# Kernel optimization log

Measured on AMD Instinct MI355X. Metric: run time of the kernel, lower is better.

The kernel has to match this reference:

```python
import jax, jax.numpy as jnp
import numpy as np

# Grid / model dims
B, H, W = 1, 90, 180
P = H * W                 # 16200 spatial points
MODEL_DIM = 130
L = MODEL_DIM - 2         # learnable_dim = 128
NH, HD = 8, 16            # n_heads, head_dim
S = 16                    # shared_hidden (DISCO out_channels)
K = 25                    # number of DISCO basis functions (piecewise-linear 5x5)
NNB = 25                  # neighbors per output point (theta_cutoff stencil)
MH = 32                   # head MLP hidden
FH = 256                  # FFN hidden


def setup_inputs() -> dict:
    key = jax.random.key(0)
    ks = jax.random.split(key, 12)
    x = jax.random.normal(ks[0], (B, H, W, MODEL_DIM), dtype=jnp.float32)
    # sparse DISCO structure: neighbor indices + precomputed (quadrature-weighted) basis values
    nbr_idx = jax.random.randint(ks[1], (P, NNB), 0, P, dtype=jnp.int32)
    basis_vals = jax.random.normal(ks[2], (K, P, NNB), dtype=jnp.float32) * 0.1
    # learnable DISCO kernel weights (out_channels=S, in_channels=1, K basis coeffs) + bias
    disco_w = jax.random.normal(ks[3], (S, K), dtype=jnp.float32) / np.sqrt(K).astype(np.float32)
    disco_b = jax.random.normal(ks[4], (S,), dtype=jnp.float32) * 0.01
    # per-head MLP params: S -> MH -> 1, one set per head
    head_w1 = jax.random.normal(ks[5], (NH, S, MH), dtype=jnp.float32) / np.sqrt(S).astype(np.float32)
    head_b1 = jnp.zeros((NH, MH), dtype=jnp.float32)
    head_w2 = jax.random.normal(ks[6], (NH, MH, 1), dtype=jnp.float32) / np.sqrt(MH).astype(np.float32)
    head_b2 = jnp.zeros((NH, 1), dtype=jnp.float32)
    # FFN: model_dim -> FH -> L, with the sin/cos input columns zeroed (as in __init__)
    ffn_w1 = jax.random.normal(ks[7], (MODEL_DIM, FH), dtype=jnp.float32) / np.sqrt(MODEL_DIM).astype(np.float32)
    ffn_w1 = ffn_w1.at[-2:, :].set(0.0)
    ffn_b1 = jnp.zeros((FH,), dtype=jnp.float32)
    ffn_w2 = jax.random.normal(ks[8], (FH, L), dtype=jnp.float32) / np.sqrt(FH).astype(np.float32)
    ffn_b2 = jnp.zeros((L,), dtype=jnp.float32)
    return dict(x=x, nbr_idx=nbr_idx, basis_vals=basis_vals, disco_w=disco_w, disco_b=disco_b,
                head_w1=head_w1, head_b1=head_b1, head_w2=head_w2, head_b2=head_b2,
                ffn_w1=ffn_w1, ffn_b1=ffn_b1, ffn_w2=ffn_w2, ffn_b2=ffn_b2)


def reference(x, nbr_idx, basis_vals, disco_w, disco_b,
              head_w1, head_b1, head_w2, head_b2,
              ffn_w1, ffn_b1, ffn_w2, ffn_b2):
    gelu = lambda t: jax.nn.gelu(t, approximate=False)  # torch nn.GELU default is exact
    x_learn = x[..., :L]          # (B,H,W,L)
    sin_cos = x[..., L:]          # (B,H,W,2)
    x_res = x_learn

    # ---- DISCO spherical conv, depthwise over B*L channels (in_channels=1) ----
    xf = jnp.transpose(x_learn, (0, 3, 1, 2)).reshape(B * L, P)      # (N, P)
    gathered = xf[:, nbr_idx]                                        # (N, P, NNB) irregular gather
    z = jnp.einsum('kpn,cpn->ckp', basis_vals, gathered)             # (N, K, P) basis projections
    y = jnp.einsum('sk,ckp->csp', disco_w, z) + disco_b[None, :, None]  # (N, S, P)
    disco_out = y.reshape(B, L, S, H, W).transpose(0, 3, 4, 1, 2)    # (B,H,W,L,S)

    # ---- per-head MLP, vectorized over heads ----
    hfeat = disco_out.reshape(B, H, W, NH, HD, S)                    # (B,H,W,NH,HD,S)
    h1 = gelu(jnp.einsum('bxyhds,hsm->bxyhdm', hfeat, head_w1) + head_b1[:, None, :])
    hout = jnp.einsum('bxyhdm,hmo->bxyhdo', h1, head_w2) + head_b2[:, None, :]  # o=1
    x_mix = hout.reshape(B, H, W, L)                                 # heads concatenated in order
    x_mix = x_mix + x_res                                            # residual

    # ---- FFN channel mixing on [x_mix, sin_cos] ----
    x_full = jnp.concatenate([x_mix, sin_cos], axis=-1)              # (B,H,W,MODEL_DIM)
    hf = gelu(jnp.einsum('bxyd,df->bxyf', x_full, ffn_w1) + ffn_b1)
    x_ffn = jnp.einsum('bxyf,fl->bxyl', hf, ffn_w2) + ffn_b2
    x_out = x_ffn + x_mix
    return jnp.concatenate([x_out, sin_cos], axis=-1)                # (B,H,W,MODEL_DIM)
```

## Files before the change

### kernel.cpp

```cpp
#include <hip/hip_runtime.h>
#include <hip/hip_bf16.h>

#define P_TOT 16200
#define MODEL_DIMC 130
#define L_DIM 128
#define NHH 8
#define S_DIM 16
#define K_DIM 25
#define NNBC 25
#define MH_DIM 32
#define FH_DIM 256

__device__ __forceinline__ float gelu_f(float x) {
    float z = fabsf(x) * 0.70710678118654752440f;
    float t = __builtin_amdgcn_rcpf(fmaf(0.3275911f, z, 1.0f));
    float poly = t * fmaf(t, fmaf(t, fmaf(t, fmaf(t, 1.061405429f, -1.453152027f),
                                          1.421413741f), -0.284496736f), 0.254829592f);
    float e = __expf(-z * z);
    float erfp = fmaf(-poly, e, 1.0f);
    float erfv = copysignf(erfp, x);
    return 0.5f * x * (1.0f + erfv);
}

#define NB1 1583
__global__ __launch_bounds__(256) void k1_bw_t(const float* __restrict__ basis,
                                               const float* __restrict__ disco_w,
                                               const float* __restrict__ hw1,
                                               float* __restrict__ bw,
                                               float* __restrict__ w1t) {
    int bid = blockIdx.x;
    int tid = threadIdx.x;
    if (bid >= NB1) {
        int i = (bid - NB1) * 256 + tid;
        if (i < NHH * S_DIM * MH_DIM) {
            int h = i >> 9, s = (i >> 5) & 15, m = i & 31;
            w1t[h * 512 + m * 16 + s] = hw1[i];
        }
        return;
    }
    __shared__ float w[S_DIM * K_DIM];
    for (int i = tid; i < S_DIM * K_DIM; i += 256) w[i] = disco_w[i];
    __syncthreads();
    int i = bid * 256 + tid;
    if (i >= P_TOT * NNBC) return;
    float bv[K_DIM];
#pragma unroll
    for (int k = 0; k < K_DIM; k++) bv[k] = basis[k * (P_TOT * NNBC) + i];
    float acc[S_DIM];
#pragma unroll
    for (int s = 0; s < S_DIM; s++) {
        float a = 0.f;
#pragma unroll
        for (int k = 0; k < K_DIM; k++) a = fmaf(w[s * K_DIM + k], bv[k], a);
        acc[s] = a;
    }
    float4* outp = (float4*)(bw + (size_t)i * S_DIM);
#pragma unroll
    for (int q = 0; q < 4; q++) {
        float4 v; v.x = acc[q*4+0]; v.y = acc[q*4+1]; v.z = acc[q*4+2]; v.w = acc[q*4+3];
        outp[q] = v;
    }
}

__global__ __launch_bounds__(256, 5) void k2_disco_head(
        const float* __restrict__ x, const int* __restrict__ nbr,
        const float* __restrict__ bw, const float* __restrict__ w1t,
        const float* __restrict__ head_b1, const float* __restrict__ head_w2,
        const float* __restrict__ head_b2, const float* __restrict__ disco_b,
        float* __restrict__ xmix) {
    __shared__ float ylds[4 * 2048];

    int tid  = threadIdx.x;
    int lane = tid & 63;
    int wv   = __builtin_amdgcn_readfirstlane(tid >> 6);
    int p0   = blockIdx.x * 4;
    int p    = p0 + wv;

    const float* bwp = bw + (size_t)p * (NNBC * S_DIM);
    const int*   nbp = nbr + p * NNBC;

    float y0[16], y1[16];
#pragma unroll
    for (int s = 0; s < 16; s++) { float db = disco_b[s]; y0[s] = db; y1[s] = db; }

    const float* xb0 = x + lane;
    const float* xb1 = x + 64 + lane;

#pragma unroll 1
    for (int nb = 0; nb < 24; nb += 2) {
        int u0 = nbp[nb], u1 = nbp[nb + 1];
        float g00 = xb0[(size_t)u0 * MODEL_DIMC];
        float g01 = xb1[(size_t)u0 * MODEL_DIMC];
        float g10 = xb0[(size_t)u1 * MODEL_DIMC];
        float g11 = xb1[(size_t)u1 * MODEL_DIMC];
#pragma unroll
        for (int s = 0; s < 16; s++) {
            float w0  = bwp[nb * 16 + s];
            float w1_ = bwp[nb * 16 + 16 + s];
            y0[s] = fmaf(g00, w0, y0[s]);
            y1[s] = fmaf(g01, w0, y1[s]);
            y0[s] = fmaf(g10, w1_, y0[s]);
            y1[s] = fmaf(g11, w1_, y1[s]);
        }
    }
    {
        int u = nbp[24];
        float g0 = xb0[(size_t)u * MODEL_DIMC];
        float g1 = xb1[(size_t)u * MODEL_DIMC];
#pragma unroll
        for (int s = 0; s < 16; s++) {
            float wv_ = bwp[24 * 16 + s];
            y0[s] = fmaf(g0, wv_, y0[s]);
            y1[s] = fmaf(g1, wv_, y1[s]);
        }
    }

    int cr0 = (lane + 8 * wv) & 127;
    int cr1 = (cr0 + 64) & 127;
#pragma unroll
    for (int s = 0; s < 16; s++) {
        ylds[wv * 2048 + s * 128 + cr0] = y0[s];
        ylds[wv * 2048 + s * 128 + cr1] = y1[s];
    }
    __syncthreads();

    int ptl = lane >> 4;
    int d   = lane & 15;
    int ybase = ptl * 2048;
    int rot   = 8 * ptl;
#pragma unroll
    for (int t = 0; t < 2; t++) {
        int hh = __builtin_amdgcn_readfirstlane(wv + 4 * t);
        int cc  = hh * 16 + d;
        int col = (cc + rot) & 127;
        float yv[16];
#pragma unroll
        for (int s = 0; s < 16; s++)
            yv[s] = ylds[ybase + s * 128 + col];
        const float* wrow = w1t + hh * (MH_DIM * S_DIM);
        const float* b1r  = head_b1 + hh * MH_DIM;
        const float* w2r  = head_w2 + hh * MH_DIM;
        float acc = head_b2[hh];
#pragma unroll 1
        for (int m = 0; m < MH_DIM; m += 2) {
            const float* wm0 = wrow + m * 16;
            const float* wm1 = wrow + m * 16 + 16;
            float a0 = b1r[m], a1 = b1r[m + 1];
            float a0b = 0.f, a1b = 0.f;
#pragma unroll
            for (int s = 0; s < 8; s++) {
                a0  = fmaf(yv[s],     wm0[s],     a0);
                a0b = fmaf(yv[s + 8], wm0[s + 8], a0b);
                a1  = fmaf(yv[s],     wm1[s],     a1);
                a1b = fmaf(yv[s + 8], wm1[s + 8], a1b);
            }
            a0 += a0b; a1 += a1b;
            a0 = gelu_f(a0);
            a1 = gelu_f(a1);
            acc = fmaf(a0, w2r[m],     acc);
            acc = fmaf(a1, w2r[m + 1], acc);
        }
        int pp = p0 + ptl;
        xmix[pp * L_DIM + cc] = acc + x[(size_t)pp * MODEL_DIMC + cc];
    }
}

__global__ __launch_bounds__(256) void k3_ffn(
        const float* __restrict__ x, const float* __restrict__ xmix,
        const float* __restrict__ w1, const float* __restrict__ b1,
        const float* __restrict__ w2, const float* __restrict__ b2,
        float* __restrict__ out) {
    __shared__ __align__(16) float xm[16 * 132];
    __shared__ __align__(16) float hfl[16 * 260];
    int tid = threadIdx.x;
    int p0 = blockIdx.x * 16;
    int valid = min(16, P_TOT - p0);
    {
        const float4* src = (const float4*)(xmix + (size_t)p0 * L_DIM);
        for (int j = tid; j < valid * 32; j += 256) {
            float4 v = src[j];
            int pt = j >> 5, q = j & 31;
            *(float4*)&xm[pt * 132 + q * 4] = v;
        }
    }
    __syncthreads();

    {
        int fid = tid & 63, wid = tid >> 6;
        int f0 = fid * 4;
        float4 bb = *(const float4*)&b1[f0];
        float acc[4][4];
#pragma unroll
        for (int i = 0; i < 4; i++) {
            acc[i][0] = bb.x; acc[i][1] = bb.y; acc[i][2] = bb.z; acc[i][3] = bb.w;
        }
#pragma unroll 2
        for (int k0 = 0; k0 < 128; k0 += 4) {
            float4 w4[4];
#pragma unroll
            for (int j = 0; j < 4; j++)
                w4[j] = *(const float4*)&w1[(k0 + j) * FH_DIM + f0];
#pragma unroll
            for (int i = 0; i < 4; i++) {
                float4 xv = *(const float4*)&xm[(wid * 4 + i) * 132 + k0];
                acc[i][0] = fmaf(xv.x, w4[0].x, acc[i][0]);
                acc[i][1] = fmaf(xv.x, w4[0].y, acc[i][1]);
                acc[i][2] = fmaf(xv.x, w4[0].z, acc[i][2]);
                acc[i][3] = fmaf(xv.x, w4[0].w, acc[i][3]);
                acc[i][0] = fmaf(xv.y, w4[1].x, acc[i][0]);
                acc[i][1] = fmaf(xv.y, w4[1].y, acc[i][1]);
                acc[i][2] = fmaf(xv.y, w4[1].z, acc[i][2]);
                acc[i][3] = fmaf(xv.y, w4[1].w, acc[i][3]);
                acc[i][0] = fmaf(xv.z, w4[2].x, acc[i][0]);
                acc[i][1] = fmaf(xv.z, w4[2].y, acc[i][1]);
                acc[i][2] = fmaf(xv.z, w4[2].z, acc[i][2]);
                acc[i][3] = fmaf(xv.z, w4[2].w, acc[i][3]);
                acc[i][0] = fmaf(xv.w, w4[3].x, acc[i][0]);
                acc[i][1] = fmaf(xv.w, w4[3].y, acc[i][1]);
                acc[i][2] = fmaf(xv.w, w4[3].z, acc[i][2]);
                acc[i][3] = fmaf(xv.w, w4[3].w, acc[i][3]);
            }
        }
#pragma unroll
        for (int i = 0; i < 4; i++) {
            int pt = wid * 4 + i;
            float4 v;
            v.x = gelu_f(acc[i][0]);
            v.y = gelu_f(acc[i][1]);
            v.z = gelu_f(acc[i][2]);
            v.w = gelu_f(acc[i][3]);
            *(float4*)&hfl[pt * 260 + f0] = v;
        }
    }
    __syncthreads();

    {
        int lid = tid & 31, pgb = tid >> 5;
        int l0 = lid * 4;
        float4 bb = *(const float4*)&b2[l0];
        float acc[2][4];
#pragma unroll
        for (int i = 0; i < 2; i++) {
            acc[i][0] = bb.x; acc[i][1] = bb.y; acc[i][2] = bb.z; acc[i][3] = bb.w;
        }
#pragma unroll 2
        for (int f0 = 0; f0 < FH_DIM; f0 += 4) {
            float4 w4[4];
#pragma unroll
            for (int j = 0; j < 4; j++)
                w4[j] = *(const float4*)&w2[(f0 + j) * L_DIM + l0];
#pragma unroll
            for (int i = 0; i < 2; i++) {
                float4 hv = *(const float4*)&hfl[(pgb * 2 + i) * 260 + f0];
                acc[i][0] = fmaf(hv.x, w4[0].x, acc[i][0]);
                acc[i][1] = fmaf(hv.x, w4[0].y, acc[i][1]);
                acc[i][2] = fmaf(hv.x, w4[0].z, acc[i][2]);
                acc[i][3] = fmaf(hv.x, w4[0].w, acc[i][3]);
                acc[i][0] = fmaf(hv.y, w4[1].x, acc[i][0]);
                acc[i][1] = fmaf(hv.y, w4[1].y, acc[i][1]);
                acc[i][2] = fmaf(hv.y, w4[1].z, acc[i][2]);
                acc[i][3] = fmaf(hv.y, w4[1].w, acc[i][3]);
                acc[i][0] = fmaf(hv.z, w4[2].x, acc[i][0]);
                acc[i][1] = fmaf(hv.z, w4[2].y, acc[i][1]);
                acc[i][2] = fmaf(hv.z, w4[2].z, acc[i][2]);
                acc[i][3] = fmaf(hv.z, w4[2].w, acc[i][3]);
                acc[i][0] = fmaf(hv.w, w4[3].x, acc[i][0]);
                acc[i][1] = fmaf(hv.w, w4[3].y, acc[i][1]);
                acc[i][2] = fmaf(hv.w, w4[3].z, acc[i][2]);
                acc[i][3] = fmaf(hv.w, w4[3].w, acc[i][3]);
            }
        }
#pragma unroll
        for (int i = 0; i < 2; i++) {
            int pl = pgb * 2 + i;
            if (pl < valid) {
                int pp = p0 + pl;
                float4 xm4 = *(const float4*)&xm[pl * 132 + l0];
                float2 o01, o23;
                o01.x = acc[i][0] + xm4.x;
                o01.y = acc[i][1] + xm4.y;
                o23.x = acc[i][2] + xm4.z;
                o23.y = acc[i][3] + xm4.w;
                *(float2*)&out[(size_t)pp * MODEL_DIMC + l0]     = o01;
                *(float2*)&out[(size_t)pp * MODEL_DIMC + l0 + 2] = o23;
            }
        }
        if (tid < 32) {
            int pt = tid >> 1, wch = tid & 1;
            if (pt < valid) {
                int pp = p0 + pt;
                out[(size_t)pp * MODEL_DIMC + 128 + wch] = x[(size_t)pp * MODEL_DIMC + 128 + wch];
            }
        }
    }
}

extern "C" void kernel_launch(void* const* d_in, const int* in_sizes, int n_in,
                              void* d_out, int out_size, void* d_ws, size_t ws_size,
                              hipStream_t stream) {
    const float* x        = (const float*)d_in[0];
    const int*   nbr      = (const int*)  d_in[1];
    const float* basis    = (const float*)d_in[2];
    const float* disco_w  = (const float*)d_in[3];
    const float* disco_b  = (const float*)d_in[4];
    const float* head_w1  = (const float*)d_in[5];
    const float* head_b1  = (const float*)d_in[6];
    const float* head_w2  = (const float*)d_in[7];
    const float* head_b2  = (const float*)d_in[8];
    const float* ffn_w1   = (const float*)d_in[9];
    const float* ffn_b1   = (const float*)d_in[10];
    const float* ffn_w2   = (const float*)d_in[11];
    const float* ffn_b2   = (const float*)d_in[12];
    float* out = (float*)d_out;

    float* bw   = (float*)d_ws;
    float* xmix = bw + (size_t)P_TOT * NNBC * S_DIM;
    float* w1t  = xmix + (size_t)P_TOT * L_DIM;

    hipLaunchKernelGGL(k1_bw_t, dim3(NB1 + 16), dim3(256), 0, stream,
                       basis, disco_w, head_w1, bw, w1t);
    hipLaunchKernelGGL(k2_disco_head, dim3(P_TOT / 4), dim3(256), 0, stream,
                       x, nbr, bw, w1t, head_b1, head_w2, head_b2, disco_b, xmix);
    hipLaunchKernelGGL(k3_ffn, dim3((P_TOT + 15) / 16), dim3(256), 0, stream,
                       x, xmix, ffn_w1, ffn_b1, ffn_w2, ffn_b2, out);
}
```

Before: 269.8 us.

## Pack x to fp16 for the gather, restructure basis-weight writes, enlarge FFN tile

The first kernel now also converts the learnable channels of x to a packed fp16 copy, staged in the output buffer, so the DISCO gather in the second kernel loads one 32-bit word (two channels) per lane instead of two fp32 loads. The gather loop is fully unrolled, preloads all neighbor indices and double-buffers gathered values in groups of five. The basis-weight kernel transposes disco_w in LDS for float4 reads and stages results through LDS for coalesced stores. The FFN kernel processes 32 points per block with launch bounds for 3 blocks per CU. The fp16 gather adds rounding error to the convolution inputs, and reusing the output buffer as scratch depends on the third kernel overwriting it completely.

```diff
diff --git a/kernel.cpp b/kernel.cpp
--- a/kernel.cpp
+++ b/kernel.cpp
@@ -1,5 +1,6 @@
 #include <hip/hip_runtime.h>
 #include <hip/hip_bf16.h>
+#include <hip/hip_fp16.h>
 
 #define P_TOT 16200
 #define MODEL_DIMC 130
@@ -23,47 +24,78 @@
 }
 
 #define NB1 1583
-__global__ __launch_bounds__(256) void k1_bw_t(const float* __restrict__ basis,
-                                               const float* __restrict__ disco_w,
-                                               const float* __restrict__ hw1,
-                                               float* __restrict__ bw,
-                                               float* __restrict__ w1t) {
+#define NPACK 1013
+__global__ __launch_bounds__(256) void k1_bw_pack(
+        const float* __restrict__ basis, const float* __restrict__ disco_w,
+        const float* __restrict__ x, const float* __restrict__ hw1,
+        float* __restrict__ bw, __half* __restrict__ xh, float* __restrict__ w1t) {
     int bid = blockIdx.x;
     int tid = threadIdx.x;
-    if (bid >= NB1) {
-        int i = (bid - NB1) * 256 + tid;
+    if (bid >= NB1 + NPACK) {
+        int i = (bid - NB1 - NPACK) * 256 + tid;
         if (i < NHH * S_DIM * MH_DIM) {
             int h = i >> 9, s = (i >> 5) & 15, m = i & 31;
             w1t[h * 512 + m * 16 + s] = hw1[i];
         }
         return;
     }
-    __shared__ float w[S_DIM * K_DIM];
-    for (int i = tid; i < S_DIM * K_DIM; i += 256) w[i] = disco_w[i];
+    if (bid >= NB1) {
+        int p0 = (bid - NB1) * 16;
+        for (int j = tid; j < 16 * 128; j += 256) {
+            int pl = j >> 7, c = j & 127;
+            int p = p0 + pl;
+            if (p < P_TOT) xh[(size_t)p * 128 + c] = __float2half(x[(size_t)p * MODEL_DIMC + c]);
+        }
+        return;
+    }
+    __shared__ float wT[K_DIM * 16];
+    __shared__ __align__(16) float st[4][64][17];
+    for (int i = tid; i < S_DIM * K_DIM; i += 256) {
+        int s = i / 25, k = i % 25;
+        wT[k * 16 + s] = disco_w[i];
+    }
     __syncthreads();
     int i = bid * 256 + tid;
-    if (i >= P_TOT * NNBC) return;
+    int ii = min(i, P_TOT * NNBC - 1);
     float bv[K_DIM];
 #pragma unroll
-    for (int k = 0; k < K_DIM; k++) bv[k] = basis[k * (P_TOT * NNBC) + i];
+    for (int k = 0; k < K_DIM; k++) bv[k] = basis[k * (P_TOT * NNBC) + ii];
     float acc[S_DIM];
 #pragma unroll
-    for (int s = 0; s < S_DIM; s++) {
-        float a = 0.f;
-#pragma unroll
-        for (int k = 0; k < K_DIM; k++) a = fmaf(w[s * K_DIM + k], bv[k], a);
-        acc[s] = a;
-    }
-    float4* outp = (float4*)(bw + (size_t)i * S_DIM);
+    for (int s = 0; s < S_DIM; s++) acc[s] = 0.f;
+    const float4* wT4 = (const float4*)wT;
+#pragma unroll
+    for (int k = 0; k < K_DIM; k++) {
+        float b = bv[k];
+        float4 w0 = wT4[k * 4 + 0], w1 = wT4[k * 4 + 1];
+        float4 w2 = wT4[k * 4 + 2], w3 = wT4[k * 4 + 3];
+        acc[0]  = fmaf(b, w0.x, acc[0]);  acc[1]  = fmaf(b, w0.y, acc[1]);
+        acc[2]  = fmaf(b, w0.z, acc[2]);  acc[3]  = fmaf(b, w0.w, acc[3]);
+        acc[4]  = fmaf(b, w1.x, acc[4]);  acc[5]  = fmaf(b, w1.y, acc[5]);
+        acc[6]  = fmaf(b, w1.z, acc[6]);  acc[7]  = fmaf(b, w1.w, acc[7]);
+        acc[8]  = fmaf(b, w2.x, acc[8]);  acc[9]  = fmaf(b, w2.y, acc[9]);
+        acc[10] = fmaf(b, w2.z, acc[10]); acc[11] = fmaf(b, w2.w, acc[11]);
+        acc[12] = fmaf(b, w3.x, acc[12]); acc[13] = fmaf(b, w3.y, acc[13]);
+        acc[14] = fmaf(b, w3.z, acc[14]); acc[15] = fmaf(b, w3.w, acc[15]);
+    }
+    int wv = tid >> 6, ln = tid & 63;
+#pragma unroll
+    for (int s = 0; s < 16; s++) st[wv][ln][s] = acc[s];
+    __builtin_amdgcn_s_waitcnt(0);
+    float4* outp4 = (float4*)bw;
+    size_t base4 = ((size_t)bid * 256 + wv * 64) * 4;
+    size_t lim4 = (size_t)P_TOT * NNBC * 4;
 #pragma unroll
     for (int q = 0; q < 4; q++) {
-        float4 v; v.x = acc[q*4+0]; v.y = acc[q*4+1]; v.z = acc[q*4+2]; v.w = acc[q*4+3];
-        outp[q] = v;
+        int g = ln + 64 * q;
+        float4 v = *(const float4*)&st[wv][g >> 2][(g & 3) * 4];
+        if (base4 + g < lim4) outp4[base4 + g] = v;
     }
 }
 
 __global__ __launch_bounds__(256, 5) void k2_disco_head(
-        const float* __restrict__ x, const int* __restrict__ nbr,
+        const float* __restrict__ x, const __half* __restrict__ xh,
+        const int* __restrict__ nbr,
         const float* __restrict__ bw, const float* __restrict__ w1t,
         const float* __restrict__ head_b1, const float* __restrict__ head_w2,
         const float* __restrict__ head_b2, const float* __restrict__ disco_b,
@@ -79,48 +111,52 @@
     const float* bwp = bw + (size_t)p * (NNBC * S_DIM);
     const int*   nbp = nbr + p * NNBC;
 
+    int un[NNBC];
+#pragma unroll
+    for (int j = 0; j < NNBC; j++) un[j] = nbp[j];
+
     float y0[16], y1[16];
 #pragma unroll
     for (int s = 0; s < 16; s++) { float db = disco_b[s]; y0[s] = db; y1[s] = db; }
 
-    const float* xb0 = x + lane;
-    const float* xb1 = x + 64 + lane;
-
-#pragma unroll 1
-    for (int nb = 0; nb < 24; nb += 2) {
-        int u0 = nbp[nb], u1 = nbp[nb + 1];
-        float g00 = xb0[(size_t)u0 * MODEL_DIMC];
-        float g01 = xb1[(size_t)u0 * MODEL_DIMC];
-        float g10 = xb0[(size_t)u1 * MODEL_DIMC];
-        float g11 = xb1[(size_t)u1 * MODEL_DIMC];
+    const uint* xbase = (const uint*)xh + lane;
+
+    uint cur[5], nxt[5];
+#pragma unroll
+    for (int j = 0; j < 5; j++) cur[j] = xbase[(size_t)un[j] * 64];
+
+#pragma unroll
+    for (int g = 0; g < 5; g++) {
+        if (g < 4) {
+#pragma unroll
+            for (int j = 0; j < 5; j++) nxt[j] = xbase[(size_t)un[(g + 1) * 5 + j] * 64];
+        }
+#pragma unroll
+        for (int j = 0; j < 5; j++) {
+            int nb = g * 5 + j;
+            __half2 h2 = *reinterpret_cast<const __half2*>(&cur[j]);
+            float ga = __low2float(h2);
+            float gb = __high2float(h2);
+#pragma unroll
+            for (int s = 0; s < 16; s++) {
+                float w = bwp[nb * 16 + s];
+                y0[s] = fmaf(ga, w, y0[s]);
+                y1[s] = fmaf(gb, w, y1[s]);
+            }
+        }
+        if (g < 4) {
+#pragma unroll
+            for (int j = 0; j < 5; j++) cur[j] = nxt[j];
+        }
+    }
+
+    {
+        int cr = (2 * lane + 8 * wv) & 127;
 #pragma unroll
         for (int s = 0; s < 16; s++) {
-            float w0  = bwp[nb * 16 + s];
-            float w1_ = bwp[nb * 16 + 16 + s];
-            y0[s] = fmaf(g00, w0, y0[s]);
-            y1[s] = fmaf(g01, w0, y1[s]);
-            y0[s] = fmaf(g10, w1_, y0[s]);
-            y1[s] = fmaf(g11, w1_, y1[s]);
-        }
-    }
-    {
-        int u = nbp[24];
-        float g0 = xb0[(size_t)u * MODEL_DIMC];
-        float g1 = xb1[(size_t)u * MODEL_DIMC];
-#pragma unroll
-        for (int s = 0; s < 16; s++) {
-            float wv_ = bwp[24 * 16 + s];
-            y0[s] = fmaf(g0, wv_, y0[s]);
-            y1[s] = fmaf(g1, wv_, y1[s]);
-        }
-    }
-
-    int cr0 = (lane + 8 * wv) & 127;
-    int cr1 = (cr0 + 64) & 127;
-#pragma unroll
-    for (int s = 0; s < 16; s++) {
-        ylds[wv * 2048 + s * 128 + cr0] = y0[s];
-        ylds[wv * 2048 + s * 128 + cr1] = y1[s];
+            float2 v; v.x = y0[s]; v.y = y1[s];
+            *(float2*)&ylds[wv * 2048 + s * 128 + cr] = v;
+        }
     }
     __syncthreads();
 
@@ -165,16 +201,16 @@
     }
 }
 
-__global__ __launch_bounds__(256) void k3_ffn(
+__global__ __launch_bounds__(256, 3) void k3_ffn(
         const float* __restrict__ x, const float* __restrict__ xmix,
         const float* __restrict__ w1, const float* __restrict__ b1,
         const float* __restrict__ w2, const float* __restrict__ b2,
         float* __restrict__ out) {
-    __shared__ __align__(16) float xm[16 * 132];
-    __shared__ __align__(16) float hfl[16 * 260];
+    __shared__ __align__(16) float xm[32 * 132];
+    __shared__ __align__(16) float hfl[32 * 260];
     int tid = threadIdx.x;
-    int p0 = blockIdx.x * 16;
-    int valid = min(16, P_TOT - p0);
+    int p0 = blockIdx.x * 32;
+    int valid = min(32, P_TOT - p0);
     {
         const float4* src = (const float4*)(xmix + (size_t)p0 * L_DIM);
         for (int j = tid; j < valid * 32; j += 256) {
@@ -189,9 +225,9 @@
         int fid = tid & 63, wid = tid >> 6;
         int f0 = fid * 4;
         float4 bb = *(const float4*)&b1[f0];
-        float acc[4][4];
-#pragma unroll
-        for (int i = 0; i < 4; i++) {
+        float acc[8][4];
+#pragma unroll
+        for (int i = 0; i < 8; i++) {
             acc[i][0] = bb.x; acc[i][1] = bb.y; acc[i][2] = bb.z; acc[i][3] = bb.w;
         }
 #pragma unroll 2
@@ -201,8 +237,8 @@
             for (int j = 0; j < 4; j++)
                 w4[j] = *(const float4*)&w1[(k0 + j) * FH_DIM + f0];
 #pragma unroll
-            for (int i = 0; i < 4; i++) {
-                float4 xv = *(const float4*)&xm[(wid * 4 + i) * 132 + k0];
+            for (int i = 0; i < 8; i++) {
+                float4 xv = *(const float4*)&xm[(wid * 8 + i) * 132 + k0];
                 acc[i][0] = fmaf(xv.x, w4[0].x, acc[i][0]);
                 acc[i][1] = fmaf(xv.x, w4[0].y, acc[i][1]);
                 acc[i][2] = fmaf(xv.x, w4[0].z, acc[i][2]);
@@ -222,8 +258,8 @@
             }
         }
 #pragma unroll
-        for (int i = 0; i < 4; i++) {
-            int pt = wid * 4 + i;
+        for (int i = 0; i < 8; i++) {
+            int pt = wid * 8 + i;
             float4 v;
             v.x = gelu_f(acc[i][0]);
             v.y = gelu_f(acc[i][1]);
@@ -238,9 +274,9 @@
         int lid = tid & 31, pgb = tid >> 5;
         int l0 = lid * 4;
         float4 bb = *(const float4*)&b2[l0];
-        float acc[2][4];
-#pragma unroll
-        for (int i = 0; i < 2; i++) {
+        float acc[4][4];
+#pragma unroll
+        for (int i = 0; i < 4; i++) {
             acc[i][0] = bb.x; acc[i][1] = bb.y; acc[i][2] = bb.z; acc[i][3] = bb.w;
         }
 #pragma unroll 2
@@ -250,29 +286,32 @@
             for (int j = 0; j < 4; j++)
                 w4[j] = *(const float4*)&w2[(f0 + j) * L_DIM + l0];
 #pragma unroll
-            for (int i = 0; i < 2; i++) {
-                float4 hv = *(const float4*)&hfl[(pgb * 2 + i) * 260 + f0];
-                acc[i][0] = fmaf(hv.x, w4[0].x, acc[i][0]);
-                acc[i][1] = fmaf(hv.x, w4[0].y, acc[i][1]);
-                acc[i][2] = fmaf(hv.x, w4[0].z, acc[i][2]);
-                acc[i][3] = fmaf(hv.x, w4[0].w, acc[i][3]);
-                acc[i][0] = fmaf(hv.y, w4[1].x, acc[i][0]);
-                acc[i][1] = fmaf(hv.y, w4[1].y, acc[i][1]);
-                acc[i][2] = fmaf(hv.y, w4[1].z, acc[i][2]);
-                acc[i][3] = fmaf(hv.y, w4[1].w, acc[i][3]);
-                acc[i][0] = fmaf(hv.z, w4[2].x, acc[i][0]);
-                acc[i][1] = fmaf(hv.z, w4[2].y, acc[i][1]);
-                acc[i][2] = fmaf(hv.z, w4[2].z, acc[i][2]);
-                acc[i][3] = fmaf(hv.z, w4[2].w, acc[i][3]);
-                acc[i][0] = fmaf(hv.w, w4[3].x, acc[i][0]);
-                acc[i][1] = fmaf(hv.w, w4[3].y, acc[i][1]);
-                acc[i][2] = fmaf(hv.w, w4[3].z, acc[i][2]);
-                acc[i][3] = fmaf(hv.w, w4[3].w, acc[i][3]);
-            }
-        }
-#pragma unroll
-        for (int i = 0; i < 2; i++) {
-            int pl = pgb * 2 + i;
+            for (int i = 0; i < 4; i++) {
+                float hv = hfl[(pgb * 4 + i) * 260 + f0];
+                float hv1 = hfl[(pgb * 4 + i) * 260 + f0 + 1];
+                float hv2 = hfl[(pgb * 4 + i) * 260 + f0 + 2];
+                float hv3 = hfl[(pgb * 4 + i) * 260 + f0 + 3];
+                acc[i][0] = fmaf(hv, w4[0].x, acc[i][0]);
+                acc[i][1] = fmaf(hv, w4[0].y, acc[i][1]);
+                acc[i][2] = fmaf(hv, w4[0].z, acc[i][2]);
+                acc[i][3] = fmaf(hv, w4[0].w, acc[i][3]);
+                acc[i][0] = fmaf(hv1, w4[1].x, acc[i][0]);
+                acc[i][1] = fmaf(hv1, w4[1].y, acc[i][1]);
+                acc[i][2] = fmaf(hv1, w4[1].z, acc[i][2]);
+                acc[i][3] = fmaf(hv1, w4[1].w, acc[i][3]);
+                acc[i][0] = fmaf(hv2, w4[2].x, acc[i][0]);
+                acc[i][1] = fmaf(hv2, w4[2].y, acc[i][1]);
+                acc[i][2] = fmaf(hv2, w4[2].z, acc[i][2]);
+                acc[i][3] = fmaf(hv2, w4[2].w, acc[i][3]);
+                acc[i][0] = fmaf(hv3, w4[3].x, acc[i][0]);
+                acc[i][1] = fmaf(hv3, w4[3].y, acc[i][1]);
+                acc[i][2] = fmaf(hv3, w4[3].z, acc[i][2]);
+                acc[i][3] = fmaf(hv3, w4[3].w, acc[i][3]);
+            }
+        }
+#pragma unroll
+        for (int i = 0; i < 4; i++) {
+            int pl = pgb * 4 + i;
             if (pl < valid) {
                 int pp = p0 + pl;
                 float4 xm4 = *(const float4*)&xm[pl * 132 + l0];
@@ -285,7 +324,7 @@
                 *(float2*)&out[(size_t)pp * MODEL_DIMC + l0 + 2] = o23;
             }
         }
-        if (tid < 32) {
+        if (tid < 64) {
             int pt = tid >> 1, wch = tid & 1;
             if (pt < valid) {
                 int pp = p0 + pt;
@@ -316,11 +355,12 @@
     float* bw   = (float*)d_ws;
     float* xmix = bw + (size_t)P_TOT * NNBC * S_DIM;
     float* w1t  = xmix + (size_t)P_TOT * L_DIM;
-
-    hipLaunchKernelGGL(k1_bw_t, dim3(NB1 + 16), dim3(256), 0, stream,
-                       basis, disco_w, head_w1, bw, w1t);
+    __half* xh  = (__half*)d_out;
+
+    hipLaunchKernelGGL(k1_bw_pack, dim3(NB1 + NPACK + 16), dim3(256), 0, stream,
+                       basis, disco_w, x, head_w1, bw, xh, w1t);
     hipLaunchKernelGGL(k2_disco_head, dim3(P_TOT / 4), dim3(256), 0, stream,
-                       x, nbr, bw, w1t, head_b1, head_w2, head_b2, disco_b, xmix);
-    hipLaunchKernelGGL(k3_ffn, dim3((P_TOT + 15) / 16), dim3(256), 0, stream,
+                       x, xh, nbr, bw, w1t, head_b1, head_w2, head_b2, disco_b, xmix);
+    hipLaunchKernelGGL(k3_ffn, dim3((P_TOT + 31) / 32), dim3(256), 0, stream,
                        x, xmix, ffn_w1, ffn_b1, ffn_w2, ffn_b2, out);
 }
```

Result: slower. 286.2 us (+6.1%).
